# Optimization experiments

Hardware: AMD Instinct MI355X
Metric: run time of the kernel (lower is better)

Reference implementation:

```python
import jax, jax.numpy as jnp
import numpy as np

DIM = 768
HEADS = 12
HEAD_DIM = DIM // HEADS


def setup_inputs() -> dict:
    key = jax.random.key(0)
    ks = jax.random.split(key, 5)
    s = 0.02
    return {
        "x": jax.random.normal(ks[0], (2, 4096, DIM), dtype=jnp.float32),
        "w_qkv": jax.random.normal(ks[1], (DIM, 3 * DIM), dtype=jnp.float32) * s,
        "b_qkv": jax.random.normal(ks[2], (3 * DIM,), dtype=jnp.float32) * s,
        "w_proj": jax.random.normal(ks[3], (DIM, DIM), dtype=jnp.float32) * s,
        "b_proj": jax.random.normal(ks[4], (DIM,), dtype=jnp.float32) * s,
    }


def reference(x, w_qkv, b_qkv, w_proj, b_proj):
    B, N, _ = x.shape
    scale = HEAD_DIM ** (-0.5)
    qkv = x @ w_qkv + b_qkv                              # [B, N, 3*DIM]
    q, k, v = jnp.split(qkv, 3, axis=-1)
    # 'b n (h d) -> b h n d'
    def to_heads(t):
        return t.reshape(B, N, HEADS, HEAD_DIM).transpose(0, 2, 1, 3)
    q, k, v = to_heads(q), to_heads(k), to_heads(v)
    attn = jnp.einsum('bhnd,bhmd->bhnm', q, k) * scale   # [B, H, N, N]
    attn = jax.nn.softmax(attn, axis=-1)
    out = jnp.einsum('bhnm,bhmd->bhnd', attn, v)         # [B, H, N, D]
    out = out.transpose(0, 2, 1, 3).reshape(B, N, DIM)   # 'b h n d -> b n (h d)'
    return out @ w_proj + b_proj
```

## Files before the change

kernel.cpp:

```cpp
#include <hip/hip_runtime.h>
#include <hip/hip_bf16.h>
#include <stdint.h>

typedef _Float16 f16x8 __attribute__((ext_vector_type(8)));
typedef _Float16 f16x4 __attribute__((ext_vector_type(4)));
typedef uint32_t u32x2 __attribute__((ext_vector_type(2)));
typedef float floatx4 __attribute__((ext_vector_type(4)));

#define NSEQ 4096
#define DIMM 768
#define NHEADS 12
#define HD 64

__device__ __forceinline__ void gload_lds16(const void* g, void* l) {
  typedef __attribute__((address_space(1))) const uint32_t GQ;
  typedef __attribute__((address_space(3))) uint32_t LQ;
  __builtin_amdgcn_global_load_lds((GQ*)g, (LQ*)l, 16, 0, 0);
}

__device__ __forceinline__ uint16_t f16_bits(float v) {
  _Float16 h = (_Float16)v;
  return __builtin_bit_cast(uint16_t, h);
}

__device__ __forceinline__ uint32_t pkrtz(float a, float b) {
  return __builtin_bit_cast(uint32_t, __builtin_amdgcn_cvt_pkrtz(a, b));
}

__device__ __forceinline__ int swz(int row, int e) {
  return row * 64 + ((((e >> 3) ^ (row & 7)) << 3) | (e & 7));
}

__global__ __launch_bounds__(256) void convert_f32_f16(
    const float4* __restrict__ src, f16x8* __restrict__ dst, int n8) {
  const int i = blockIdx.x * 256 + threadIdx.x;
  if (i >= n8) return;
  const float4 a = src[2 * i], b = src[2 * i + 1];
  f16x8 o;
  o[0] = (_Float16)a.x; o[1] = (_Float16)a.y; o[2] = (_Float16)a.z; o[3] = (_Float16)a.w;
  o[4] = (_Float16)b.x; o[5] = (_Float16)b.y; o[6] = (_Float16)b.z; o[7] = (_Float16)b.w;
  dst[i] = o;
}

__global__ __launch_bounds__(256) void transpose_f32_f16(
    const float* __restrict__ src, uint16_t* __restrict__ dst, int R, int C) {
  __shared__ uint16_t tile[32][33];
  const int c0 = blockIdx.x * 32, r0 = blockIdx.y * 32;
  const int tx = threadIdx.x, ty = threadIdx.y;
#pragma unroll
  for (int i = 0; i < 32; i += 8)
    tile[ty + i][tx] = f16_bits(src[(size_t)(r0 + ty + i) * C + (c0 + tx)]);
  __syncthreads();
#pragma unroll
  for (int i = 0; i < 32; i += 8)
    dst[(size_t)(c0 + ty + i) * R + (r0 + tx)] = tile[tx][ty + i];
}

__global__ __launch_bounds__(256) void transpose_b16(
    const uint16_t* __restrict__ src, uint16_t* __restrict__ dst, int R, int C) {
  __shared__ uint16_t tile[32][33];
  const size_t plane = (size_t)blockIdx.z * (size_t)R * (size_t)C;
  const int c0 = blockIdx.x * 32, r0 = blockIdx.y * 32;
  const int tx = threadIdx.x, ty = threadIdx.y;
#pragma unroll
  for (int i = 0; i < 32; i += 8)
    tile[ty + i][tx] = src[plane + (size_t)(r0 + ty + i) * C + (c0 + tx)];
  __syncthreads();
#pragma unroll
  for (int i = 0; i < 32; i += 8)
    dst[plane + (size_t)(c0 + ty + i) * R + (r0 + tx)] = tile[tx][ty + i];
}

__global__ __launch_bounds__(256) void gemm_bt(
    const _Float16* __restrict__ A, const _Float16* __restrict__ Bt,
    const float* __restrict__ bias, int K, int mode,
    void* __restrict__ o0, _Float16* __restrict__ o1, _Float16* __restrict__ o2) {
  __shared__ __attribute__((aligned(16))) _Float16 As[128 * 32];
  __shared__ __attribute__((aligned(16))) _Float16 Bs[128 * 32];
  __shared__ float bias_s[128];
  const int tid = threadIdx.x;
  const int wv = tid >> 6;
  const int lane = tid & 63;
  const int quad = lane >> 4, l16 = lane & 15;
  const int wm = (wv >> 1) * 64, wn = (wv & 1) * 64;
  const int m0 = blockIdx.y * 128, n0 = blockIdx.x * 128;

  if (tid < 128) bias_s[tid] = bias[n0 + tid];

  floatx4 acc[4][4];
#pragma unroll
  for (int i = 0; i < 4; ++i)
#pragma unroll
    for (int j = 0; j < 4; ++j) acc[i][j] = (floatx4){0.f, 0.f, 0.f, 0.f};

  const int gr = lane >> 2, gc = (lane & 3) * 8;
  const _Float16* Ag = A + (size_t)(m0 + wv * 32 + gr) * K + gc;
  const _Float16* Bg = Bt + (size_t)(n0 + wv * 32 + gr) * K + gc;
  const size_t K16 = (size_t)16 * K;
  _Float16* As0 = &As[wv * 1024];
  _Float16* Bs0 = &Bs[wv * 1024];

  for (int kt = 0; kt < K; kt += 32) {
    __syncthreads();
    gload_lds16(Ag + kt, As0);
    gload_lds16(Ag + kt + K16, As0 + 512);
    gload_lds16(Bg + kt, Bs0);
    gload_lds16(Bg + kt + K16, Bs0 + 512);
    __syncthreads();
    f16x8 af[4], bfr[4];
#pragma unroll
    for (int i = 0; i < 4; ++i)
      af[i] = *(const f16x8*)&As[(wm + i * 16 + l16) * 32 + quad * 8];
#pragma unroll
    for (int j = 0; j < 4; ++j)
      bfr[j] = *(const f16x8*)&Bs[(wn + j * 16 + l16) * 32 + quad * 8];
#pragma unroll
    for (int i = 0; i < 4; ++i)
#pragma unroll
      for (int j = 0; j < 4; ++j)
        acc[i][j] = __builtin_amdgcn_mfma_f32_16x16x32_f16(af[i], bfr[j], acc[i][j], 0, 0, 0);
  }

  if (mode == 0) {
    float* of = (float*)o0;
#pragma unroll
    for (int i = 0; i < 4; ++i)
#pragma unroll
      for (int j = 0; j < 4; ++j) {
        const int col = n0 + wn + j * 16 + l16;
        const float b = bias_s[wn + j * 16 + l16];
        const int mrow = m0 + wm + i * 16 + quad * 4;
#pragma unroll
        for (int r = 0; r < 4; ++r)
          of[(size_t)(mrow + r) * DIMM + col] = acc[i][j][r] + b;
      }
  } else {
    const int sec = n0 / DIMM;
    _Float16* dst = (sec == 0) ? (_Float16*)o0 : (sec == 1) ? o1 : o2;
    const float sc = (sec == 0) ? 0.18033688011112042f : 1.0f;
#pragma unroll
    for (int i = 0; i < 4; ++i)
#pragma unroll
      for (int j = 0; j < 4; ++j) {
        const int n = n0 + wn + j * 16 + l16;
        const int c = n - sec * DIMM;
        const int h = c >> 6, d = c & 63;
        const float b = bias_s[wn + j * 16 + l16];
        const int mrow = m0 + wm + i * 16 + quad * 4;
#pragma unroll
        for (int r = 0; r < 4; ++r) {
          const int m = mrow + r;
          const int bb = m >> 12, nr = m & 4095;
          dst[(((size_t)(bb * NHEADS + h)) * NSEQ + nr) * HD + d] =
              (_Float16)((acc[i][j][r] + b) * sc);
        }
      }
  }
}

__global__ __launch_bounds__(256, 3) void attn(
    const _Float16* __restrict__ Qg, const _Float16* __restrict__ Kg,
    const _Float16* __restrict__ VTg, _Float16* __restrict__ ctx) {
  __shared__ __attribute__((aligned(16))) _Float16 Pt[128 * 64];
  __shared__ __attribute__((aligned(16))) _Float16 Ks[2][64 * 64];
  __shared__ __attribute__((aligned(16))) _Float16 VTs[2][64 * 64];
  const int tid = threadIdx.x;
  const int wv = tid >> 6, lane = tid & 63;
  const int quad = lane >> 4, l16 = lane & 15;
  const int bi = blockIdx.x;
  const int xcd = bi & 7, j = bi >> 3;
  const int bh = xcd * 3 + (j >> 5);
  const int q0 = (j & 31) * 128;
  const int bb = bh / NHEADS, h = bh - bb * NHEADS;
  const _Float16* Qp = Qg + (size_t)bh * NSEQ * HD;
  const _Float16* Kp = Kg + (size_t)bh * NSEQ * HD;
  const _Float16* VTp = VTg + (size_t)bh * HD * NSEQ;

  const int krow = tid >> 3;
  const int kcol = (((tid & 7) ^ ((tid >> 3) & 7)) * 8);
  const int l7 = l16 & 7;

#pragma unroll
  for (int i = 0; i < 4; ++i)
    gload_lds16(Qp + (size_t)(q0 + i * 32 + krow) * HD + kcol, &Pt[(i * 256 + wv * 64) * 8]);
#pragma unroll
  for (int i = 0; i < 2; ++i) {
    gload_lds16(Kp + (size_t)(i * 32 + krow) * HD + kcol, &Ks[0][(i * 256 + wv * 64) * 8]);
    gload_lds16(VTp + (size_t)(i * 32 + krow) * NSEQ + kcol, &VTs[0][(i * 256 + wv * 64) * 8]);
  }
  __syncthreads();

  f16x8 aq[2][2];
#pragma unroll
  for (int it = 0; it < 2; ++it)
#pragma unroll
    for (int ks = 0; ks < 2; ++ks)
      aq[it][ks] = *(const f16x8*)&Pt[swz(wv * 32 + it * 16 + l16, ks * 32 + quad * 8)];

#pragma unroll
  for (int i = 0; i < 2; ++i) {
    gload_lds16(Kp + (size_t)(64 + i * 32 + krow) * HD + kcol, &Ks[1][(i * 256 + wv * 64) * 8]);
    gload_lds16(VTp + (size_t)(i * 32 + krow) * NSEQ + 64 + kcol, &VTs[1][(i * 256 + wv * 64) * 8]);
  }

  floatx4 o[2][4];
  float lp[2] = {0.f, 0.f};
#pragma unroll
  for (int it = 0; it < 2; ++it)
#pragma unroll
    for (int jn = 0; jn < 4; ++jn) o[it][jn] = (floatx4){0.f, 0.f, 0.f, 0.f};

  const int prow = wv * 32 + l16;
  f16x8 vr[2][4];

  auto QKT = [&](const _Float16* bK, floatx4 (&s)[2][4]) {
#pragma unroll
    for (int ks = 0; ks < 2; ++ks) {
#pragma unroll
      for (int im = 0; im < 4; ++im) {
        const f16x8 bk = *(const f16x8*)&bK[swz(im * 16 + l16, ks * 32 + quad * 8)];
        s[0][im] = __builtin_amdgcn_mfma_f32_16x16x32_f16(bk, aq[0][ks], s[0][im], 0, 0, 0);
        s[1][im] = __builtin_amdgcn_mfma_f32_16x16x32_f16(bk, aq[1][ks], s[1][im], 0, 0, 0);
      }
    }
  };
  auto LDVR = [&](const _Float16* bV) {
#pragma unroll
    for (int kk = 0; kk < 2; ++kk)
#pragma unroll
      for (int jn = 0; jn < 4; ++jn)
        vr[kk][jn] = *(const f16x8*)&bV[swz(jn * 16 + l16, kk * 32 + quad * 8)];
  };
  auto SMAX = [&](floatx4 (&s)[2][4]) {
#pragma unroll
    for (int it = 0; it < 2; ++it) {
      const int row = prow + it * 16;
#pragma unroll
      for (int im = 0; im < 4; ++im) {
        float p0 = __builtin_amdgcn_exp2f(s[it][im][0]);
        float p1 = __builtin_amdgcn_exp2f(s[it][im][1]);
        float p2 = __builtin_amdgcn_exp2f(s[it][im][2]);
        float p3 = __builtin_amdgcn_exp2f(s[it][im][3]);
        lp[it] += (p0 + p1) + (p2 + p3);
        const u32x2 packed = {pkrtz(p0, p1), pkrtz(p2, p3)};
        *(f16x4*)&Pt[row * 64 + (((im * 2 + (quad >> 1)) ^ l7) << 3) + (quad & 1) * 4] =
            __builtin_bit_cast(f16x4, packed);
      }
    }
  };
  auto LDAP = [&](f16x8 (&ap)[2][2]) {
#pragma unroll
    for (int kk = 0; kk < 2; ++kk) {
      ap[kk][0] = *(const f16x8*)&Pt[swz(prow, kk * 32 + quad * 8)];
      ap[kk][1] = *(const f16x8*)&Pt[swz(prow + 16, kk * 32 + quad * 8)];
    }
  };
  auto PV = [&](const f16x8 (&ap)[2][2]) {
#pragma unroll
    for (int kk = 0; kk < 2; ++kk) {
#pragma unroll
      for (int jn = 0; jn < 4; ++jn) {
        o[0][jn] = __builtin_amdgcn_mfma_f32_16x16x32_f16(ap[kk][0], vr[kk][jn], o[0][jn], 0, 0, 0);
        o[1][jn] = __builtin_amdgcn_mfma_f32_16x16x32_f16(ap[kk][1], vr[kk][jn], o[1][jn], 0, 0, 0);
      }
    }
  };

  {
    floatx4 s[2][4];
#pragma unroll
    for (int it = 0; it < 2; ++it)
#pragma unroll
      for (int im = 0; im < 4; ++im) s[it][im] = (floatx4){0.f, 0.f, 0.f, 0.f};
    __builtin_amdgcn_s_setprio(1);
    QKT(Ks[0], s);
    __builtin_amdgcn_s_setprio(0);
    LDVR(VTs[0]);
    SMAX(s);
  }

  auto REGION = [&](const _Float16* bK, const _Float16* bV,
                    _Float16* wK, _Float16* wV, int kvn, bool dodma) {
    __syncthreads();
    if (dodma) {
#pragma unroll
      for (int i = 0; i < 2; ++i) {
        gload_lds16(Kp + (size_t)(kvn + i * 32 + krow) * HD + kcol, &wK[(i * 256 + wv * 64) * 8]);
        gload_lds16(VTp + (size_t)(i * 32 + krow) * NSEQ + kvn + kcol, &wV[(i * 256 + wv * 64) * 8]);
      }
    }
    f16x8 ap[2][2];
    LDAP(ap);
    floatx4 s[2][4];
#pragma unroll
    for (int it = 0; it < 2; ++it)
#pragma unroll
      for (int im = 0; im < 4; ++im) s[it][im] = (floatx4){0.f, 0.f, 0.f, 0.f};
    __builtin_amdgcn_s_setprio(1);
    QKT(bK, s);
    PV(ap);
    __builtin_amdgcn_s_setprio(0);
    LDVR(bV);
    SMAX(s);
  };

#pragma unroll 1
  for (int p = 0; p < 31; ++p) {
    const int t0 = 2 * p + 1;
    REGION(Ks[1], VTs[1], Ks[0], VTs[0], (t0 + 1) * 64, true);
    REGION(Ks[0], VTs[0], Ks[1], VTs[1], (t0 + 2) * 64, true);
  }
  REGION(Ks[1], VTs[1], Ks[0], VTs[0], 0, false);
  {
    f16x8 ap[2][2];
    LDAP(ap);
    PV(ap);
  }

#pragma unroll
  for (int it = 0; it < 2; ++it) {
    lp[it] += __shfl_xor(lp[it], 16);
    lp[it] += __shfl_xor(lp[it], 32);
  }
#pragma unroll
  for (int it = 0; it < 2; ++it)
#pragma unroll
    for (int r = 0; r < 4; ++r) {
      const int q = q0 + wv * 32 + it * 16 + quad * 4 + r;
      const float lq = __shfl(lp[it], (lane & 48) | (quad * 4 + r));
      const float inv = 1.0f / lq;
      _Float16* dst = ctx + (size_t)(bb * NSEQ + q) * DIMM + h * HD;
#pragma unroll
      for (int jn = 0; jn < 4; ++jn)
        dst[jn * 16 + l16] = (_Float16)(o[it][jn][r] * inv);
    }
}

extern "C" void kernel_launch(void* const* d_in, const int* in_sizes, int n_in,
                              void* d_out, int out_size, void* d_ws, size_t ws_size,
                              hipStream_t stream) {
  char* ws = (char*)d_ws;
  _Float16* xc = (_Float16*)ws;      ws += (size_t)8192 * 768 * 2;
  _Float16* wqkvT = (_Float16*)ws;   ws += (size_t)2304 * 768 * 2;
  _Float16* wprojT = (_Float16*)ws;  ws += (size_t)768 * 768 * 2;
  const size_t qkv_elems = (size_t)2 * NHEADS * NSEQ * HD;
  _Float16* Qb = (_Float16*)ws;      ws += qkv_elems * 2;
  _Float16* Kb = (_Float16*)ws;      ws += qkv_elems * 2;
  _Float16* Vb = (_Float16*)ws;      ws += qkv_elems * 2;
  _Float16* VTb = (_Float16*)ws;     ws += qkv_elems * 2;
  _Float16* ctx = xc;

  const dim3 tb(32, 8, 1);
  const dim3 b256(256, 1, 1);
  hipLaunchKernelGGL(convert_f32_f16, dim3(3072, 1, 1), b256, 0, stream,
                     (const float4*)d_in[0], (f16x8*)xc, 8192 * 768 / 8);
  hipLaunchKernelGGL(transpose_f32_f16, dim3(72, 24, 1), tb, 0, stream,
                     (const float*)d_in[1], (uint16_t*)wqkvT, 768, 2304);
  hipLaunchKernelGGL(transpose_f32_f16, dim3(24, 24, 1), tb, 0, stream,
                     (const float*)d_in[3], (uint16_t*)wprojT, 768, 768);
  hipLaunchKernelGGL(gemm_bt, dim3(18, 64, 1), b256, 0, stream,
                     xc, wqkvT, (const float*)d_in[2], 768, 1, (void*)Qb, Kb, Vb);
  hipLaunchKernelGGL(transpose_b16, dim3(2, 128, 24), tb, 0, stream,
                     (const uint16_t*)Vb, (uint16_t*)VTb, 4096, 64);
  hipLaunchKernelGGL(attn, dim3(768, 1, 1), b256, 0, stream, Qb, Kb, VTb, ctx);
  hipLaunchKernelGGL(gemm_bt, dim3(6, 64, 1), b256, 0, stream,
                     ctx, wprojT, (const float*)d_in[4], 768, 0, d_out,
                     (_Float16*)nullptr, (_Float16*)nullptr);
}
```

Measured before the change: 281.8 us.

## Triple-buffer GEMM loads, stream V from global, compute row sums via MFMA

The projection GEMM moves from a single-buffered loop with two barriers per step to a three-stage LDS ring using vmcnt waits and one barrier per step, with MFMA priority raised. The aim is to overlap global-to-LDS loads with compute. In attention, V^T tiles are now read straight from global memory into registers instead of being staged in LDS, which cuts LDS traffic and size and may allow higher occupancy. The softmax row sum is now computed by an extra MFMA against a ones vector, replacing the per-lane exp additions and cross-lane shuffles. In exchange, V reads become uncoalesced, latency-exposed global loads, and the row-sum accumulation now runs on the FP16-rounded probabilities.

After: 363.3 us. 1.29x slower.

```diff
diff --git a/kernel.cpp b/kernel.cpp
--- a/kernel.cpp
+++ b/kernel.cpp
@@ -75,8 +75,8 @@
     const _Float16* __restrict__ A, const _Float16* __restrict__ Bt,
     const float* __restrict__ bias, int K, int mode,
     void* __restrict__ o0, _Float16* __restrict__ o1, _Float16* __restrict__ o2) {
-  __shared__ __attribute__((aligned(16))) _Float16 As[128 * 32];
-  __shared__ __attribute__((aligned(16))) _Float16 Bs[128 * 32];
+  __shared__ __attribute__((aligned(16))) _Float16 As[3][128 * 32];
+  __shared__ __attribute__((aligned(16))) _Float16 Bs[3][128 * 32];
   __shared__ float bias_s[128];
   const int tid = threadIdx.x;
   const int wv = tid >> 6;
@@ -97,29 +97,51 @@
   const _Float16* Ag = A + (size_t)(m0 + wv * 32 + gr) * K + gc;
   const _Float16* Bg = Bt + (size_t)(n0 + wv * 32 + gr) * K + gc;
   const size_t K16 = (size_t)16 * K;
-  _Float16* As0 = &As[wv * 1024];
-  _Float16* Bs0 = &Bs[wv * 1024];
-
-  for (int kt = 0; kt < K; kt += 32) {
-    __syncthreads();
+
+  auto STAGE = [&](int buf, int kt) {
+    _Float16* As0 = &As[buf][wv * 1024];
+    _Float16* Bs0 = &Bs[buf][wv * 1024];
     gload_lds16(Ag + kt, As0);
     gload_lds16(Ag + kt + K16, As0 + 512);
     gload_lds16(Bg + kt, Bs0);
     gload_lds16(Bg + kt + K16, Bs0 + 512);
-    __syncthreads();
+  };
+  auto COMPUTE = [&](int buf) {
     f16x8 af[4], bfr[4];
 #pragma unroll
     for (int i = 0; i < 4; ++i)
-      af[i] = *(const f16x8*)&As[(wm + i * 16 + l16) * 32 + quad * 8];
+      af[i] = *(const f16x8*)&As[buf][(wm + i * 16 + l16) * 32 + quad * 8];
 #pragma unroll
     for (int j = 0; j < 4; ++j)
-      bfr[j] = *(const f16x8*)&Bs[(wn + j * 16 + l16) * 32 + quad * 8];
+      bfr[j] = *(const f16x8*)&Bs[buf][(wn + j * 16 + l16) * 32 + quad * 8];
+    __builtin_amdgcn_s_setprio(1);
 #pragma unroll
     for (int i = 0; i < 4; ++i)
 #pragma unroll
       for (int j = 0; j < 4; ++j)
         acc[i][j] = __builtin_amdgcn_mfma_f32_16x16x32_f16(af[i], bfr[j], acc[i][j], 0, 0, 0);
-  }
+    __builtin_amdgcn_s_setprio(0);
+  };
+
+  STAGE(0, 0);
+  STAGE(1, 32);
+  const int nt = K >> 5;
+  int b0 = 0, b1 = 1, b2 = 2;
+#pragma unroll 1
+  for (int t = 0; t < nt - 2; ++t) {
+    asm volatile("s_waitcnt vmcnt(4)" ::: "memory");
+    __builtin_amdgcn_s_barrier();
+    STAGE(b2, (t + 2) * 32);
+    COMPUTE(b0);
+    const int tmp = b0; b0 = b1; b1 = b2; b2 = tmp;
+  }
+  asm volatile("s_waitcnt vmcnt(4)" ::: "memory");
+  __builtin_amdgcn_s_barrier();
+  COMPUTE(b0);
+  b0 = b1;
+  asm volatile("s_waitcnt vmcnt(0)" ::: "memory");
+  __builtin_amdgcn_s_barrier();
+  COMPUTE(b0);
 
   if (mode == 0) {
     float* of = (float*)o0;
@@ -163,7 +185,6 @@
     const _Float16* __restrict__ VTg, _Float16* __restrict__ ctx) {
   __shared__ __attribute__((aligned(16))) _Float16 Pt[128 * 64];
   __shared__ __attribute__((aligned(16))) _Float16 Ks[2][64 * 64];
-  __shared__ __attribute__((aligned(16))) _Float16 VTs[2][64 * 64];
   const int tid = threadIdx.x;
   const int wv = tid >> 6, lane = tid & 63;
   const int quad = lane >> 4, l16 = lane & 15;
@@ -184,10 +205,8 @@
   for (int i = 0; i < 4; ++i)
     gload_lds16(Qp + (size_t)(q0 + i * 32 + krow) * HD + kcol, &Pt[(i * 256 + wv * 64) * 8]);
 #pragma unroll
-  for (int i = 0; i < 2; ++i) {
+  for (int i = 0; i < 2; ++i)
     gload_lds16(Kp + (size_t)(i * 32 + krow) * HD + kcol, &Ks[0][(i * 256 + wv * 64) * 8]);
-    gload_lds16(VTp + (size_t)(i * 32 + krow) * NSEQ + kcol, &VTs[0][(i * 256 + wv * 64) * 8]);
-  }
   __syncthreads();
 
   f16x8 aq[2][2];
@@ -198,21 +217,33 @@
       aq[it][ks] = *(const f16x8*)&Pt[swz(wv * 32 + it * 16 + l16, ks * 32 + quad * 8)];
 
 #pragma unroll
-  for (int i = 0; i < 2; ++i) {
+  for (int i = 0; i < 2; ++i)
     gload_lds16(Kp + (size_t)(64 + i * 32 + krow) * HD + kcol, &Ks[1][(i * 256 + wv * 64) * 8]);
-    gload_lds16(VTp + (size_t)(i * 32 + krow) * NSEQ + 64 + kcol, &VTs[1][(i * 256 + wv * 64) * 8]);
-  }
+
+  f16x8 ones;
+#pragma unroll
+  for (int e = 0; e < 8; ++e) ones[e] = (_Float16)1.0f;
 
   floatx4 o[2][4];
-  float lp[2] = {0.f, 0.f};
-#pragma unroll
-  for (int it = 0; it < 2; ++it)
+  floatx4 lacc[2];
+#pragma unroll
+  for (int it = 0; it < 2; ++it) {
+    lacc[it] = (floatx4){0.f, 0.f, 0.f, 0.f};
 #pragma unroll
     for (int jn = 0; jn < 4; ++jn) o[it][jn] = (floatx4){0.f, 0.f, 0.f, 0.f};
+  }
 
   const int prow = wv * 32 + l16;
   f16x8 vr[2][4];
 
+  auto VLOAD = [&](int vn) {
+    const _Float16* vp = VTp + vn;
+#pragma unroll
+    for (int kk = 0; kk < 2; ++kk)
+#pragma unroll
+      for (int jn = 0; jn < 4; ++jn)
+        vr[kk][jn] = *(const f16x8*)(vp + (size_t)(jn * 16 + l16) * NSEQ + kk * 32 + quad * 8);
+  };
   auto QKT = [&](const _Float16* bK, floatx4 (&s)[2][4]) {
 #pragma unroll
     for (int ks = 0; ks < 2; ++ks) {
@@ -223,13 +254,6 @@
         s[1][im] = __builtin_amdgcn_mfma_f32_16x16x32_f16(bk, aq[1][ks], s[1][im], 0, 0, 0);
       }
     }
-  };
-  auto LDVR = [&](const _Float16* bV) {
-#pragma unroll
-    for (int kk = 0; kk < 2; ++kk)
-#pragma unroll
-      for (int jn = 0; jn < 4; ++jn)
-        vr[kk][jn] = *(const f16x8*)&bV[swz(jn * 16 + l16, kk * 32 + quad * 8)];
   };
   auto SMAX = [&](floatx4 (&s)[2][4]) {
 #pragma unroll
@@ -241,7 +265,6 @@
         float p1 = __builtin_amdgcn_exp2f(s[it][im][1]);
         float p2 = __builtin_amdgcn_exp2f(s[it][im][2]);
         float p3 = __builtin_amdgcn_exp2f(s[it][im][3]);
-        lp[it] += (p0 + p1) + (p2 + p3);
         const u32x2 packed = {pkrtz(p0, p1), pkrtz(p2, p3)};
         *(f16x4*)&Pt[row * 64 + (((im * 2 + (quad >> 1)) ^ l7) << 3) + (quad & 1) * 4] =
             __builtin_bit_cast(f16x4, packed);
@@ -258,6 +281,8 @@
   auto PV = [&](const f16x8 (&ap)[2][2]) {
 #pragma unroll
     for (int kk = 0; kk < 2; ++kk) {
+      lacc[0] = __builtin_amdgcn_mfma_f32_16x16x32_f16(ap[kk][0], ones, lacc[0], 0, 0, 0);
+      lacc[1] = __builtin_amdgcn_mfma_f32_16x16x32_f16(ap[kk][1], ones, lacc[1], 0, 0, 0);
 #pragma unroll
       for (int jn = 0; jn < 4; ++jn) {
         o[0][jn] = __builtin_amdgcn_mfma_f32_16x16x32_f16(ap[kk][0], vr[kk][jn], o[0][jn], 0, 0, 0);
@@ -265,6 +290,8 @@
       }
     }
   };
+
+  VLOAD(0);
 
   {
     floatx4 s[2][4];
@@ -275,19 +302,16 @@
     __builtin_amdgcn_s_setprio(1);
     QKT(Ks[0], s);
     __builtin_amdgcn_s_setprio(0);
-    LDVR(VTs[0]);
     SMAX(s);
   }
 
-  auto REGION = [&](const _Float16* bK, const _Float16* bV,
-                    _Float16* wK, _Float16* wV, int kvn, bool dodma) {
+  auto REGION = [&](const _Float16* bK, _Float16* wK, int t, bool dodma) {
     __syncthreads();
     if (dodma) {
-#pragma unroll
-      for (int i = 0; i < 2; ++i) {
+      const int kvn = ((t + 1) & 63) * 64;
+#pragma unroll
+      for (int i = 0; i < 2; ++i)
         gload_lds16(Kp + (size_t)(kvn + i * 32 + krow) * HD + kcol, &wK[(i * 256 + wv * 64) * 8]);
-        gload_lds16(VTp + (size_t)(i * 32 + krow) * NSEQ + kvn + kcol, &wV[(i * 256 + wv * 64) * 8]);
-      }
     }
     f16x8 ap[2][2];
     LDAP(ap);
@@ -300,17 +324,17 @@
     QKT(bK, s);
     PV(ap);
     __builtin_amdgcn_s_setprio(0);
-    LDVR(bV);
+    VLOAD(t * 64);
     SMAX(s);
   };
 
 #pragma unroll 1
   for (int p = 0; p < 31; ++p) {
-    const int t0 = 2 * p + 1;
-    REGION(Ks[1], VTs[1], Ks[0], VTs[0], (t0 + 1) * 64, true);
-    REGION(Ks[0], VTs[0], Ks[1], VTs[1], (t0 + 2) * 64, true);
-  }
-  REGION(Ks[1], VTs[1], Ks[0], VTs[0], 0, false);
+    const int t = 2 * p + 1;
+    REGION(Ks[1], Ks[0], t, true);
+    REGION(Ks[0], Ks[1], t + 1, true);
+  }
+  REGION(Ks[1], Ks[0], 63, false);
   {
     f16x8 ap[2][2];
     LDAP(ap);
@@ -318,17 +342,11 @@
   }
 
 #pragma unroll
-  for (int it = 0; it < 2; ++it) {
-    lp[it] += __shfl_xor(lp[it], 16);
-    lp[it] += __shfl_xor(lp[it], 32);
-  }
-#pragma unroll
   for (int it = 0; it < 2; ++it)
 #pragma unroll
     for (int r = 0; r < 4; ++r) {
       const int q = q0 + wv * 32 + it * 16 + quad * 4 + r;
-      const float lq = __shfl(lp[it], (lane & 48) | (quad * 4 + r));
-      const float inv = 1.0f / lq;
+      const float inv = 1.0f / lacc[it][r];
       _Float16* dst = ctx + (size_t)(bb * NSEQ + q) * DIMM + h * HD;
 #pragma unroll
       for (int jn = 0; jn < 4; ++jn)
```

## Triple-buffer GEMM LDS loads with prefetch and raised MFMA priority

Applied to the files above, without the earlier changes.

The gemm_bt kernel now keeps three LDS buffers for A and B tiles and prefetches the K-tile two steps ahead with global_load_lds, waiting with vmcnt(4) and a single barrier per iteration instead of two syncthreads. This is meant to overlap global-to-LDS transfers with MFMA compute in the QKV and output-projection GEMMs. It also raises wave priority around the MFMA block. LDS use grows threefold, which can lower occupancy, and the relaxed synchronisation relies on the vmcnt ordering being correct.

Result: no change. 286.2 us (+1.6%).

```diff
diff --git a/kernel.cpp b/kernel.cpp
--- a/kernel.cpp
+++ b/kernel.cpp
@@ -75,8 +75,8 @@
     const _Float16* __restrict__ A, const _Float16* __restrict__ Bt,
     const float* __restrict__ bias, int K, int mode,
     void* __restrict__ o0, _Float16* __restrict__ o1, _Float16* __restrict__ o2) {
-  __shared__ __attribute__((aligned(16))) _Float16 As[128 * 32];
-  __shared__ __attribute__((aligned(16))) _Float16 Bs[128 * 32];
+  __shared__ __attribute__((aligned(16))) _Float16 As[3][128 * 32];
+  __shared__ __attribute__((aligned(16))) _Float16 Bs[3][128 * 32];
   __shared__ float bias_s[128];
   const int tid = threadIdx.x;
   const int wv = tid >> 6;
@@ -97,29 +97,51 @@
   const _Float16* Ag = A + (size_t)(m0 + wv * 32 + gr) * K + gc;
   const _Float16* Bg = Bt + (size_t)(n0 + wv * 32 + gr) * K + gc;
   const size_t K16 = (size_t)16 * K;
-  _Float16* As0 = &As[wv * 1024];
-  _Float16* Bs0 = &Bs[wv * 1024];
-
-  for (int kt = 0; kt < K; kt += 32) {
-    __syncthreads();
+
+  auto STAGE = [&](int buf, int kt) {
+    _Float16* As0 = &As[buf][wv * 1024];
+    _Float16* Bs0 = &Bs[buf][wv * 1024];
     gload_lds16(Ag + kt, As0);
     gload_lds16(Ag + kt + K16, As0 + 512);
     gload_lds16(Bg + kt, Bs0);
     gload_lds16(Bg + kt + K16, Bs0 + 512);
-    __syncthreads();
+  };
+  auto COMPUTE = [&](int buf) {
     f16x8 af[4], bfr[4];
 #pragma unroll
     for (int i = 0; i < 4; ++i)
-      af[i] = *(const f16x8*)&As[(wm + i * 16 + l16) * 32 + quad * 8];
+      af[i] = *(const f16x8*)&As[buf][(wm + i * 16 + l16) * 32 + quad * 8];
 #pragma unroll
     for (int j = 0; j < 4; ++j)
-      bfr[j] = *(const f16x8*)&Bs[(wn + j * 16 + l16) * 32 + quad * 8];
+      bfr[j] = *(const f16x8*)&Bs[buf][(wn + j * 16 + l16) * 32 + quad * 8];
+    __builtin_amdgcn_s_setprio(1);
 #pragma unroll
     for (int i = 0; i < 4; ++i)
 #pragma unroll
       for (int j = 0; j < 4; ++j)
         acc[i][j] = __builtin_amdgcn_mfma_f32_16x16x32_f16(af[i], bfr[j], acc[i][j], 0, 0, 0);
-  }
+    __builtin_amdgcn_s_setprio(0);
+  };
+
+  STAGE(0, 0);
+  STAGE(1, 32);
+  const int nt = K >> 5;
+  int b0 = 0, b1 = 1, b2 = 2;
+#pragma unroll 1
+  for (int t = 0; t < nt - 2; ++t) {
+    asm volatile("s_waitcnt vmcnt(4)" ::: "memory");
+    __builtin_amdgcn_s_barrier();
+    STAGE(b2, (t + 2) * 32);
+    COMPUTE(b0);
+    const int tmp = b0; b0 = b1; b1 = b2; b2 = tmp;
+  }
+  asm volatile("s_waitcnt vmcnt(4)" ::: "memory");
+  __builtin_amdgcn_s_barrier();
+  COMPUTE(b0);
+  b0 = b1;
+  asm volatile("s_waitcnt vmcnt(0)" ::: "memory");
+  __builtin_amdgcn_s_barrier();
+  COMPUTE(b0);
 
   if (mode == 0) {
     float* of = (float*)o0;
```
